# Optimization experiments

Measured on AMD Instinct MI355X. Metric: run time of the kernel, lower is better.

The kernel has to match this reference:

```python
import jax, jax.numpy as jnp
import numpy as np

NUM_HEADER = 8
DIM_HIDDEN = 512
DIM_HEADER = DIM_HIDDEN // NUM_HEADER


def setup_inputs() -> dict:
    key = jax.random.key(0)
    ks = jax.random.split(key, 11)
    B, S, D = 2, 4096, DIM_HIDDEN
    scale = 1.0 / np.sqrt(D)
    inp = {
        "q": jax.random.normal(ks[0], (B, S, D), jnp.float32),
        "k": jax.random.normal(ks[1], (B, S, D), jnp.float32),
        "v": jax.random.normal(ks[2], (B, S, D), jnp.float32),
        # nn.Linear weights are [out, in]; y = x @ W.T + b
        "Wq": jax.random.normal(ks[3], (D, D), jnp.float32) * scale,
        "bq": jax.random.normal(ks[4], (D,), jnp.float32) * scale,
        "Wk": jax.random.normal(ks[5], (D, D), jnp.float32) * scale,
        "bk": jax.random.normal(ks[6], (D,), jnp.float32) * scale,
        "Wv": jax.random.normal(ks[7], (D, D), jnp.float32) * scale,
        "bv": jax.random.normal(ks[8], (D,), jnp.float32) * scale,
        "Wo": jax.random.normal(ks[9], (D, D), jnp.float32) * scale,
        "bo": jax.random.normal(ks[10], (D,), jnp.float32) * scale,
    }
    return inp


def reference(q, k, v, Wq, bq, Wk, bk, Wv, bv, Wo, bo):
    B = q.shape[0]
    H, dh = NUM_HEADER, DIM_HEADER

    def proj(x, W, b):
        # [B,S,D] -> [B,H,S,dh]
        y = jnp.einsum('bsd,ed->bse', x, W) + b
        return y.reshape(B, -1, H, dh).transpose(0, 2, 1, 3)

    qh = proj(q, Wq, bq)
    kh = proj(k, Wk, bk)
    vh = proj(v, Wv, bv)

    scores = jnp.einsum('bhqd,bhkd->bhqk', qh, kh) / jnp.sqrt(jnp.float32(dh))
    attn = jax.nn.softmax(scores, axis=-1)
    ctx = jnp.einsum('bhqk,bhkd->bhqd', attn, vh)
    concat = ctx.transpose(0, 2, 1, 3).reshape(B, -1, H * dh)
    return jnp.einsum('bsd,ed->bse', concat, Wo) + bo
```

## Files before the change

kernel.cpp:

```cpp
#include <hip/hip_runtime.h>
#include <hip/hip_bf16.h>

typedef __attribute__((ext_vector_type(8))) short short8;
typedef __attribute__((ext_vector_type(4))) float f32x4;
typedef __attribute__((ext_vector_type(16))) float f32x16;
typedef __attribute__((ext_vector_type(4))) float f4v;

#define SEQ 4096
#define NBH 16
#define SCALE_Q 0.18033688011112042f

#define MFMA16(a, b, c) __builtin_amdgcn_mfma_f32_16x16x32_bf16(a, b, c, 0, 0, 0)
#define MFMA32(a, b, c) __builtin_amdgcn_mfma_f32_32x32x16_bf16(a, b, c, 0, 0, 0)

__device__ __forceinline__ short f2bf(float f) {
  union { float f; unsigned u; } x; x.f = f;
  unsigned r = x.u + 0x7FFFu + ((x.u >> 16) & 1u);
  return (short)(r >> 16);
}

__device__ __forceinline__ unsigned cvt_pk_bf16(float lo, float hi) {
  unsigned r;
  asm("v_cvt_pk_bf16_f32 %0, %1, %2" : "=v"(r) : "v"(lo), "v"(hi));
  return r;
}

__device__ __forceinline__ short8 cvt8(const float* __restrict__ src) {
  f4v v0 = *(const f4v*)src;
  f4v v1 = *(const f4v*)(src + 4);
  union { unsigned u[4]; short8 s; } r;
  r.u[0] = cvt_pk_bf16(v0[0], v0[1]);
  r.u[1] = cvt_pk_bf16(v0[2], v0[3]);
  r.u[2] = cvt_pk_bf16(v1[0], v1[1]);
  r.u[3] = cvt_pk_bf16(v1[2], v1[3]);
  return r.s;
}

__device__ __forceinline__ void gll16(const void* g, void* l) {
  __builtin_amdgcn_global_load_lds(
      (const __attribute__((address_space(1))) void*)g,
      (__attribute__((address_space(3))) void*)l, 16, 0, 0);
}

__device__ __forceinline__ void pswap(unsigned& a, unsigned& b) {
  asm volatile("v_permlane32_swap_b32 %0, %1" : "+v"(a), "+v"(b));
}

#define SBAR()                              \
  __builtin_amdgcn_sched_barrier(0);        \
  __builtin_amdgcn_s_barrier();             \
  __builtin_amdgcn_sched_barrier(0)

__global__ __launch_bounds__(256) void cvt_w(
    const float* __restrict__ w0, const float* __restrict__ w1,
    const float* __restrict__ w2, const float* __restrict__ w3,
    short* __restrict__ dst)
{
  int i = blockIdx.x * 256 + threadIdx.x;
  int m = i >> 15;
  int off = (i & 32767) * 8;
  const float* s = (m == 0) ? w0 : (m == 1) ? w1 : (m == 2) ? w2 : w3;
  *(short8*)(dst + (size_t)m * 262144 + off) = cvt8(s + off);
}

template <bool SWAP>
__device__ __forceinline__ void qkv_kloop(
    const float* __restrict__ Af, const short* __restrict__ W,
    char* smemA, char* smemB, f32x4 (&acc)[4][2],
    int tile_m, int tile_n, int t, int g, int q, int w)
{
  short (*As)[72] = (short(*)[72])smemA;
  for (int k0 = 0; k0 < 512; k0 += 64) {
    __syncthreads();
#pragma unroll
    for (int it = 0; it < 2; ++it) {
      int i = it * 256 + t;
      int r = i >> 3, sg = i & 7;
      *(short8*)&As[r][sg * 8] =
          cvt8(Af + (size_t)(tile_m + r) * 512 + k0 + sg * 8);
    }
#pragma unroll
    for (int it = 0; it < 4; ++it) {
      int i = it * 256 + t;
      int row = i >> 3, cg = i & 7;
      const char* gp = (const char*)W +
          ((size_t)(tile_n + row) * 512 + k0) * 2 + ((cg ^ (row & 7)) << 4);
      gll16(gp, smemB + (size_t)(it * 256 + (t & ~63)) * 16);
    }
    __syncthreads();
#pragma unroll
    for (int kk = 0; kk < 2; ++kk) {
      short8 af[4], bfv[2];
#pragma unroll
      for (int mi = 0; mi < 4; ++mi)
        af[mi] = *(const short8*)&As[mi * 16 + q][kk * 32 + g * 8];
#pragma unroll
      for (int ni = 0; ni < 2; ++ni) {
        int rB = w * 32 + ni * 16 + q;
        bfv[ni] = *(const short8*)(smemB + rB * 128 +
                                   (((4 * kk + g) ^ (rB & 7)) << 4));
      }
#pragma unroll
      for (int mi = 0; mi < 4; ++mi)
#pragma unroll
        for (int ni = 0; ni < 2; ++ni) {
          if (SWAP)
            acc[mi][ni] = MFMA16(bfv[ni], af[mi], acc[mi][ni]);
          else
            acc[mi][ni] = MFMA16(af[mi], bfv[ni], acc[mi][ni]);
        }
    }
  }
}

__global__ __launch_bounds__(256) void qkv_gemm(
    const float* __restrict__ qin, const float* __restrict__ kin,
    const float* __restrict__ vin, const short* __restrict__ Wb,
    const float* __restrict__ bq, const float* __restrict__ bk,
    const float* __restrict__ bv,
    short* __restrict__ Qh, short* __restrict__ Kh, short* __restrict__ Vt)
{
  __shared__ __align__(16) char smemA[64 * 72 * 2];
  __shared__ __align__(16) char smemB[128 * 64 * 2];
  const int t    = threadIdx.x;
  const int lane = t & 63;
  const int w    = t >> 6;
  const int g    = lane >> 4;
  const int q    = lane & 15;
  const int tile_n = blockIdx.x * 128;
  const int tile_m = blockIdx.y * 64;
  const int z      = blockIdx.z;

  const float* Af   = (z == 0) ? qin : (z == 1) ? kin : vin;
  const float* bias = (z == 0) ? bq  : (z == 1) ? bk  : bv;
  const short* W    = Wb + (size_t)z * 262144;

  f32x4 acc[4][2];
#pragma unroll
  for (int mi = 0; mi < 4; ++mi)
#pragma unroll
    for (int ni = 0; ni < 2; ++ni)
#pragma unroll
      for (int j = 0; j < 4; ++j) acc[mi][ni][j] = 0.f;

  if (z == 2)
    qkv_kloop<true>(Af, W, smemA, smemB, acc, tile_m, tile_n, t, g, q, w);
  else
    qkv_kloop<false>(Af, W, smemA, smemB, acc, tile_m, tile_n, t, g, q, w);

#pragma unroll
  for (int mi = 0; mi < 4; ++mi) {
#pragma unroll
    for (int ni = 0; ni < 2; ++ni) {
#pragma unroll
      for (int j = 0; j < 4; ++j) {
        if (z == 2) {
          int e = tile_n + w * 32 + ni * 16 + 4 * g + j;
          int srow = tile_m + mi * 16 + q;
          float val = acc[mi][ni][j] + bias[e];
          int b = srow >> 12, sl = srow & 4095;
          int h = e >> 6, d = e & 63;
          Vt[((size_t)((b * 8 + h) * 64 + d)) * SEQ + sl] = f2bf(val);
        } else {
          int m = tile_m + mi * 16 + g * 4 + j;
          int e = tile_n + w * 32 + ni * 16 + q;
          float val = acc[mi][ni][j] + bias[e];
          int b = m >> 12, s = m & 4095;
          int h = e >> 6, d = e & 63;
          size_t off = ((size_t)(b * 8 + h) * SEQ + s) * 64 + d;
          if (z == 0) Qh[off] = f2bf(val * SCALE_Q);
          else        Kh[off] = f2bf(val);
        }
      }
    }
  }
}

template <int MODE>
__global__ __launch_bounds__(256) void gemm_bt(
    const short* __restrict__ Ab,
    const short* __restrict__ Wb, const float* __restrict__ bias,
    const float* __restrict__ Opart, const float* __restrict__ lsum,
    void* __restrict__ Cout)
{
  __shared__ __align__(16) char smemA[64 * 72 * 2];
  __shared__ __align__(16) char smemB[128 * 64 * 2];
  const int t    = threadIdx.x;
  const int lane = t & 63;
  const int w    = t >> 6;
  const int g    = lane >> 4;
  const int q    = lane & 15;
  const int tile_n = blockIdx.x * 128;
  const int tile_m = blockIdx.y * 64;

  f32x4 acc[4][2];
#pragma unroll
  for (int mi = 0; mi < 4; ++mi)
#pragma unroll
    for (int ni = 0; ni < 2; ++ni)
#pragma unroll
      for (int j = 0; j < 4; ++j) acc[mi][ni][j] = 0.f;

  for (int k0 = 0; k0 < 512; k0 += 64) {
    __syncthreads();
    if (MODE == 3) {
#pragma unroll
      for (int it = 0; it < 2; ++it) {
        int i = it * 256 + t;
        int row = i >> 3, cg = i & 7;
        const char* gp = (const char*)Ab +
            ((size_t)(tile_m + row) * 512 + k0) * 2 + ((cg ^ (row & 7)) << 4);
        gll16(gp, smemA + (size_t)(it * 256 + (t & ~63)) * 16);
      }
    } else {
#pragma unroll
      for (int it = 0; it < 2; ++it) {
        int i = it * 256 + t;
        int row = i >> 3, cg = i & 7;
        int cgs = cg ^ (row & 7);
        int m = tile_m + row;
        int b = m >> 12, s = m & 4095;
        int h = k0 >> 6;
        size_t g0 = (size_t)(b * 8 + h) * SEQ + s;
        float inv = 1.0f / (lsum[g0] + lsum[g0 + (size_t)NBH * SEQ]);
        const float* o0 = Opart + g0 * 64 + cgs * 8;
        const float* o1 = Opart + (g0 + (size_t)NBH * SEQ) * 64 + cgs * 8;
        f4v a0 = *(const f4v*)o0, a1 = *(const f4v*)(o0 + 4);
        f4v b0 = *(const f4v*)o1, b1 = *(const f4v*)(o1 + 4);
        float vv[8];
#pragma unroll
        for (int j = 0; j < 4; ++j) vv[j] = (a0[j] + b0[j]) * inv;
#pragma unroll
        for (int j = 0; j < 4; ++j) vv[4 + j] = (a1[j] + b1[j]) * inv;
        union { unsigned u[4]; short8 s8; } r;
        r.u[0] = cvt_pk_bf16(vv[0], vv[1]);
        r.u[1] = cvt_pk_bf16(vv[2], vv[3]);
        r.u[2] = cvt_pk_bf16(vv[4], vv[5]);
        r.u[3] = cvt_pk_bf16(vv[6], vv[7]);
        *(short8*)(smemA + (size_t)i * 16) = r.s8;
      }
    }
#pragma unroll
    for (int it = 0; it < 4; ++it) {
      int i = it * 256 + t;
      int row = i >> 3, cg = i & 7;
      const char* gp = (const char*)Wb +
          ((size_t)(tile_n + row) * 512 + k0) * 2 + ((cg ^ (row & 7)) << 4);
      gll16(gp, smemB + (size_t)(it * 256 + (t & ~63)) * 16);
    }
    __syncthreads();
#pragma unroll
    for (int kk = 0; kk < 2; ++kk) {
      short8 af[4], bfv[2];
#pragma unroll
      for (int mi = 0; mi < 4; ++mi) {
        int rA = mi * 16 + q;
        af[mi] = *(const short8*)(smemA + rA * 128 +
                                  (((4 * kk + g) ^ (rA & 7)) << 4));
      }
#pragma unroll
      for (int ni = 0; ni < 2; ++ni) {
        int rB = w * 32 + ni * 16 + q;
        bfv[ni] = *(const short8*)(smemB + rB * 128 +
                                   (((4 * kk + g) ^ (rB & 7)) << 4));
      }
#pragma unroll
      for (int mi = 0; mi < 4; ++mi)
#pragma unroll
        for (int ni = 0; ni < 2; ++ni)
          acc[mi][ni] = MFMA16(af[mi], bfv[ni], acc[mi][ni]);
    }
  }

#pragma unroll
  for (int mi = 0; mi < 4; ++mi) {
#pragma unroll
    for (int ni = 0; ni < 2; ++ni) {
#pragma unroll
      for (int j = 0; j < 4; ++j) {
        int m = tile_m + mi * 16 + g * 4 + j;
        int e = tile_n + w * 32 + ni * 16 + q;
        ((float*)Cout)[(size_t)m * 512 + e] = acc[mi][ni][j] + bias[e];
      }
    }
  }
}

template <int NSPLIT>
__global__ __launch_bounds__(256, 4) void attn_kernel(
    const short* __restrict__ Qh, const short* __restrict__ Kh,
    const short* __restrict__ Vt, short* __restrict__ ctx,
    float* __restrict__ Opart, float* __restrict__ lsum)
{
  __shared__ __align__(16) char smem[2][16384];
  const int t    = threadIdx.x;
  const int lane = t & 63;
  const int w    = t >> 6;
  const int l31  = lane & 31;
  const int hi   = lane >> 5;

  const int fid = blockIdx.x;
  int qt, bh, split;
  if (NSPLIT == 1) {
    int lid = (fid & 7) * 64 + (fid >> 3);
    qt = lid & 31; bh = lid >> 5; split = 0;
  } else {
    int lid = (fid & 7) * 128 + (fid >> 3);
    qt = lid & 31; split = (lid >> 5) & 1; bh = lid >> 6;
  }
  const int NT  = (SEQ / 64) / NSPLIT;
  const int kt0 = split * NT;

  const size_t kbase = (size_t)bh * SEQ * 64;
  const size_t vbase = (size_t)bh * 64 * SEQ;
  const int q0 = qt * 128 + w * 32;

  short8 qf[4];
#pragma unroll
  for (int m = 0; m < 4; ++m)
    qf[m] = *(const short8*)(Qh + kbase + (size_t)(q0 + l31) * 64 + m * 16 + hi * 8);

  f32x16 fz;
#pragma unroll
  for (int r = 0; r < 16; ++r) fz[r] = 0.f;
  f32x16 acc0 = fz, acc1 = fz;
  float lrun = 0.f;

  const int rif  = lane >> 3;
  const int scol = ((lane & 7) ^ rif) * 16;
  const int xr   = (hi * 16) ^ ((lane & 7) << 4);

#define STAGE(buf, kt)                                                         \
  {                                                                            \
    _Pragma("unroll")                                                          \
    for (int i = 0; i < 4; ++i) {                                              \
      int c = w * 4 + i;                                                       \
      char* ldst = &smem[buf][c * 1024];                                       \
      if (c < 8) {                                                             \
        int row = c * 8 + rif;                                                 \
        const char* gp = (const char*)Kh +                                     \
            ((kbase + (size_t)((kt) * 64 + row) * 64) * 2 + scol);             \
        gll16(gp, ldst);                                                       \
      } else {                                                                 \
        int row = (c - 8) * 8 + rif;                                           \
        const char* gp = (const char*)Vt +                                     \
            ((vbase + (size_t)row * SEQ + (kt) * 64) * 2 + scol);              \
        gll16(gp, ldst);                                                       \
      }                                                                        \
    }                                                                          \
  }

  STAGE(0, kt0);
  int cur = 0;

  for (int it = 0; it < NT; ++it) {
    const int kt = kt0 + it;
    asm volatile("s_waitcnt vmcnt(0)" ::: "memory");
    SBAR();
    if (it < NT - 1) STAGE(cur ^ 1, kt + 1);

    const char* Kb = &smem[cur][0];
    const char* Vb = &smem[cur][8192];

    f32x16 s0, s1;
    {
      short8 k0 = *(const short8*)(Kb + (size_t)(l31) * 128 + ((32 * 0) ^ xr));
      short8 k1 = *(const short8*)(Kb + (size_t)(32 + l31) * 128 + ((32 * 0) ^ xr));
      __builtin_amdgcn_s_setprio(1);
      s0 = MFMA32(k0, qf[0], fz);
      s1 = MFMA32(k1, qf[0], fz);
      __builtin_amdgcn_s_setprio(0);
    }
#pragma unroll
    for (int m = 1; m < 4; ++m) {
      short8 k0 = *(const short8*)(Kb + (size_t)(l31) * 128 + ((32 * m) ^ xr));
      short8 k1 = *(const short8*)(Kb + (size_t)(32 + l31) * 128 + ((32 * m) ^ xr));
      __builtin_amdgcn_s_setprio(1);
      s0 = MFMA32(k0, qf[m], s0);
      s1 = MFMA32(k1, qf[m], s1);
      __builtin_amdgcn_s_setprio(0);
    }

#pragma unroll
    for (int r = 0; r < 16; ++r) s0[r] = __builtin_amdgcn_exp2f(s0[r]);
    float rs0;
    {
      float b_[8];
#pragma unroll
      for (int r = 0; r < 8; ++r) b_[r] = s0[r] + s0[r + 8];
#pragma unroll
      for (int r = 0; r < 4; ++r) b_[r] += b_[r + 4];
      rs0 = (b_[0] + b_[1]) + (b_[2] + b_[3]);
    }
    union { unsigned u[4]; short8 v; } A0c, A1c;
    {
      unsigned p0 = cvt_pk_bf16(s0[0], s0[1]);
      unsigned p1 = cvt_pk_bf16(s0[2], s0[3]);
      unsigned p2 = cvt_pk_bf16(s0[4], s0[5]);
      unsigned p3 = cvt_pk_bf16(s0[6], s0[7]);
      unsigned p4 = cvt_pk_bf16(s0[8], s0[9]);
      unsigned p5 = cvt_pk_bf16(s0[10], s0[11]);
      unsigned p6 = cvt_pk_bf16(s0[12], s0[13]);
      unsigned p7 = cvt_pk_bf16(s0[14], s0[15]);
      pswap(p0, p2); pswap(p1, p3); pswap(p4, p6); pswap(p5, p7);
      A0c.u[0] = p0; A0c.u[1] = p1; A0c.u[2] = p2; A0c.u[3] = p3;
      A1c.u[0] = p4; A1c.u[1] = p5; A1c.u[2] = p6; A1c.u[3] = p7;
    }
#pragma unroll
    for (int h2 = 0; h2 < 2; ++h2) {
      short8 pa = h2 ? A1c.v : A0c.v;
      short8 vf0 = *(const short8*)(Vb + (size_t)(l31) * 128 + ((32 * h2) ^ xr));
      short8 vf1 = *(const short8*)(Vb + (size_t)(32 + l31) * 128 + ((32 * h2) ^ xr));
      __builtin_amdgcn_s_setprio(1);
      acc0 = MFMA32(pa, vf0, acc0);
      acc1 = MFMA32(pa, vf1, acc1);
      __builtin_amdgcn_s_setprio(0);
    }

#pragma unroll
    for (int r = 0; r < 16; ++r) s1[r] = __builtin_amdgcn_exp2f(s1[r]);
    float rs1;
    {
      float b_[8];
#pragma unroll
      for (int r = 0; r < 8; ++r) b_[r] = s1[r] + s1[r + 8];
#pragma unroll
      for (int r = 0; r < 4; ++r) b_[r] += b_[r + 4];
      rs1 = (b_[0] + b_[1]) + (b_[2] + b_[3]);
    }
    {
      unsigned p0 = cvt_pk_bf16(s1[0], s1[1]);
      unsigned p1 = cvt_pk_bf16(s1[2], s1[3]);
      unsigned p2 = cvt_pk_bf16(s1[4], s1[5]);
      unsigned p3 = cvt_pk_bf16(s1[6], s1[7]);
      unsigned p4 = cvt_pk_bf16(s1[8], s1[9]);
      unsigned p5 = cvt_pk_bf16(s1[10], s1[11]);
      unsigned p6 = cvt_pk_bf16(s1[12], s1[13]);
      unsigned p7 = cvt_pk_bf16(s1[14], s1[15]);
      pswap(p0, p2); pswap(p1, p3); pswap(p4, p6); pswap(p5, p7);
      A0c.u[0] = p0; A0c.u[1] = p1; A0c.u[2] = p2; A0c.u[3] = p3;
      A1c.u[0] = p4; A1c.u[1] = p5; A1c.u[2] = p6; A1c.u[3] = p7;
    }
#pragma unroll
    for (int h2 = 0; h2 < 2; ++h2) {
      short8 pa = h2 ? A1c.v : A0c.v;
      short8 vf0 = *(const short8*)(Vb + (size_t)(l31) * 128 + ((64 + 32 * h2) ^ xr));
      short8 vf1 = *(const short8*)(Vb + (size_t)(32 + l31) * 128 + ((64 + 32 * h2) ^ xr));
      __builtin_amdgcn_s_setprio(1);
      acc0 = MFMA32(pa, vf0, acc0);
      acc1 = MFMA32(pa, vf1, acc1);
      __builtin_amdgcn_s_setprio(0);
    }

    float rs = rs0 + rs1;
    rs += __shfl_xor(rs, 32);
    lrun += rs;

    cur ^= 1;
  }

  if (NSPLIT == 1) {
    const int b = bh >> 3, hh = bh & 7;
    const float inv = 1.0f / lrun;
#pragma unroll
    for (int r = 0; r < 16; ++r) {
      int ql = (r & 3) + 8 * (r >> 2) + 4 * hi;
      float iv = __shfl(inv, ql);
      int qrow = q0 + ql;
      size_t off = ((size_t)(b * SEQ + qrow)) * 512 + hh * 64 + l31;
      ctx[off]      = f2bf(acc0[r] * iv);
      ctx[off + 32] = f2bf(acc1[r] * iv);
    }
  } else {
    float* Ob = Opart + (((size_t)(split * NBH + bh) * SEQ + q0)) * 64;
#pragma unroll
    for (int r = 0; r < 16; ++r) {
      int ql = (r & 3) + 8 * (r >> 2) + 4 * hi;
      Ob[(size_t)ql * 64 + l31]      = acc0[r];
      Ob[(size_t)ql * 64 + l31 + 32] = acc1[r];
    }
    if (hi == 0)
      lsum[(size_t)(split * NBH + bh) * SEQ + q0 + l31] = lrun;
  }
}

extern "C" void kernel_launch(void* const* d_in, const int* in_sizes, int n_in,
                              void* d_out, int out_size, void* d_ws, size_t ws_size,
                              hipStream_t stream) {
  const float* q  = (const float*)d_in[0];
  const float* k  = (const float*)d_in[1];
  const float* v  = (const float*)d_in[2];
  const float* Wq = (const float*)d_in[3];
  const float* bq = (const float*)d_in[4];
  const float* Wk = (const float*)d_in[5];
  const float* bk = (const float*)d_in[6];
  const float* Wv = (const float*)d_in[7];
  const float* bv = (const float*)d_in[8];
  const float* Wo = (const float*)d_in[9];
  const float* bo = (const float*)d_in[10];

  const size_t NELT = (size_t)NBH * SEQ * 64;
  short* Qh  = (short*)d_ws;
  short* Kh  = Qh + NELT;
  short* Vt  = Kh + NELT;
  short* ctx = Vt + NELT;
  short* Wb  = ctx + NELT;
  float* Opart = (float*)(Wb + 4 * 262144);
  float* lsum  = Opart + 2 * (size_t)NBH * SEQ * 64;
  const char* ws_end = (const char*)(lsum + 2 * (size_t)NBH * SEQ);
  const bool split2 = ws_size >= (size_t)(ws_end - (const char*)d_ws);

  dim3 tb(256);
  cvt_w<<<dim3(512), tb, 0, stream>>>(Wq, Wk, Wv, Wo, Wb);

  qkv_gemm<<<dim3(4, 128, 3), tb, 0, stream>>>(q, k, v, Wb, bq, bk, bv,
                                               Qh, Kh, Vt);
  if (split2) {
    attn_kernel<2><<<dim3(1024), tb, 0, stream>>>(Qh, Kh, Vt, ctx, Opart, lsum);
    gemm_bt<4><<<dim3(4, 128), tb, 0, stream>>>(nullptr, Wb + 786432, bo, Opart, lsum, d_out);
  } else {
    attn_kernel<1><<<dim3(512), tb, 0, stream>>>(Qh, Kh, Vt, ctx, Opart, lsum);
    gemm_bt<3><<<dim3(4, 128), tb, 0, stream>>>(ctx, Wb + 786432, bo, nullptr, nullptr, d_out);
  }
}
```

Baseline: 163.2 us.

## Split attention KV range four ways and store partial outputs in bf16

Raises the attention split-K factor from 2 to 4, launching 2048 blocks instead of 1024 so the GPU holds more parallel work. Partial outputs are now written as bf16 rather than fp32, which keeps the intermediate traffic roughly unchanged despite twice as many partials. The output projection sums four partials and their row sums. This adds combine work and a rounding step on unnormalized partial accumulators, and the workspace layout is reorganized so the partials alias the ctx buffer.

```diff
diff --git a/kernel.cpp b/kernel.cpp
--- a/kernel.cpp
+++ b/kernel.cpp
@@ -17,6 +17,12 @@
   union { float f; unsigned u; } x; x.f = f;
   unsigned r = x.u + 0x7FFFu + ((x.u >> 16) & 1u);
   return (short)(r >> 16);
+}
+
+__device__ __forceinline__ float bf2f(short s) {
+  union { unsigned u; float f; } x;
+  x.u = ((unsigned)(unsigned short)s) << 16;
+  return x.f;
 }
 
 __device__ __forceinline__ unsigned cvt_pk_bf16(float lo, float hi) {
@@ -180,7 +186,7 @@
 __global__ __launch_bounds__(256) void gemm_bt(
     const short* __restrict__ Ab,
     const short* __restrict__ Wb, const float* __restrict__ bias,
-    const float* __restrict__ Opart, const float* __restrict__ lsum,
+    const short* __restrict__ OpartB, const float* __restrict__ lsum,
     void* __restrict__ Cout)
 {
   __shared__ __align__(16) char smemA[64 * 72 * 2];
@@ -221,17 +227,24 @@
         int m = tile_m + row;
         int b = m >> 12, s = m & 4095;
         int h = k0 >> 6;
-        size_t g0 = (size_t)(b * 8 + h) * SEQ + s;
-        float inv = 1.0f / (lsum[g0] + lsum[g0 + (size_t)NBH * SEQ]);
-        const float* o0 = Opart + g0 * 64 + cgs * 8;
-        const float* o1 = Opart + (g0 + (size_t)NBH * SEQ) * 64 + cgs * 8;
-        f4v a0 = *(const f4v*)o0, a1 = *(const f4v*)(o0 + 4);
-        f4v b0 = *(const f4v*)o1, b1 = *(const f4v*)(o1 + 4);
+        size_t base = (size_t)(b * 8 + h) * SEQ + s;
+        float ltot = 0.f;
+#pragma unroll
+        for (int sp = 0; sp < 4; ++sp)
+          ltot += lsum[base + (size_t)sp * NBH * SEQ];
+        float inv = 1.0f / ltot;
         float vv[8];
 #pragma unroll
-        for (int j = 0; j < 4; ++j) vv[j] = (a0[j] + b0[j]) * inv;
-#pragma unroll
-        for (int j = 0; j < 4; ++j) vv[4 + j] = (a1[j] + b1[j]) * inv;
+        for (int j = 0; j < 8; ++j) vv[j] = 0.f;
+#pragma unroll
+        for (int sp = 0; sp < 4; ++sp) {
+          short8 o = *(const short8*)(OpartB +
+              (base + (size_t)sp * NBH * SEQ) * 64 + cgs * 8);
+#pragma unroll
+          for (int j = 0; j < 8; ++j) vv[j] += bf2f(o[j]);
+        }
+#pragma unroll
+        for (int j = 0; j < 8; ++j) vv[j] *= inv;
         union { unsigned u[4]; short8 s8; } r;
         r.u[0] = cvt_pk_bf16(vv[0], vv[1]);
         r.u[1] = cvt_pk_bf16(vv[2], vv[3]);
@@ -290,7 +303,7 @@
 __global__ __launch_bounds__(256, 4) void attn_kernel(
     const short* __restrict__ Qh, const short* __restrict__ Kh,
     const short* __restrict__ Vt, short* __restrict__ ctx,
-    float* __restrict__ Opart, float* __restrict__ lsum)
+    short* __restrict__ OpartB, float* __restrict__ lsum)
 {
   __shared__ __align__(16) char smem[2][16384];
   const int t    = threadIdx.x;
@@ -305,8 +318,8 @@
     int lid = (fid & 7) * 64 + (fid >> 3);
     qt = lid & 31; bh = lid >> 5; split = 0;
   } else {
-    int lid = (fid & 7) * 128 + (fid >> 3);
-    qt = lid & 31; split = (lid >> 5) & 1; bh = lid >> 6;
+    int lid = (fid & 7) * 256 + (fid >> 3);
+    qt = lid & 31; split = (lid >> 5) & 3; bh = lid >> 7;
   }
   const int NT  = (SEQ / 64) / NSPLIT;
   const int kt0 = split * NT;
@@ -472,12 +485,12 @@
       ctx[off + 32] = f2bf(acc1[r] * iv);
     }
   } else {
-    float* Ob = Opart + (((size_t)(split * NBH + bh) * SEQ + q0)) * 64;
+    short* Ob = OpartB + ((size_t)(split * NBH + bh) * SEQ + q0) * 64;
 #pragma unroll
     for (int r = 0; r < 16; ++r) {
       int ql = (r & 3) + 8 * (r >> 2) + 4 * hi;
-      Ob[(size_t)ql * 64 + l31]      = acc0[r];
-      Ob[(size_t)ql * 64 + l31 + 32] = acc1[r];
+      Ob[(size_t)ql * 64 + l31]      = f2bf(acc0[r]);
+      Ob[(size_t)ql * 64 + l31 + 32] = f2bf(acc1[r]);
     }
     if (hi == 0)
       lsum[(size_t)(split * NBH + bh) * SEQ + q0 + l31] = lrun;
@@ -503,23 +516,23 @@
   short* Qh  = (short*)d_ws;
   short* Kh  = Qh + NELT;
   short* Vt  = Kh + NELT;
-  short* ctx = Vt + NELT;
-  short* Wb  = ctx + NELT;
-  float* Opart = (float*)(Wb + 4 * 262144);
-  float* lsum  = Opart + 2 * (size_t)NBH * SEQ * 64;
-  const char* ws_end = (const char*)(lsum + 2 * (size_t)NBH * SEQ);
-  const bool split2 = ws_size >= (size_t)(ws_end - (const char*)d_ws);
+  short* ctx    = Vt + NELT;
+  short* OpartB = ctx;
+  short* Wb     = OpartB + 4 * NELT;
+  float* lsum   = (float*)(Wb + 4 * 262144);
+  const char* ws_end = (const char*)(lsum + 4 * (size_t)NBH * SEQ);
+  const bool split4 = ws_size >= (size_t)(ws_end - (const char*)d_ws);
 
   dim3 tb(256);
   cvt_w<<<dim3(512), tb, 0, stream>>>(Wq, Wk, Wv, Wo, Wb);
 
   qkv_gemm<<<dim3(4, 128, 3), tb, 0, stream>>>(q, k, v, Wb, bq, bk, bv,
                                                Qh, Kh, Vt);
-  if (split2) {
-    attn_kernel<2><<<dim3(1024), tb, 0, stream>>>(Qh, Kh, Vt, ctx, Opart, lsum);
-    gemm_bt<4><<<dim3(4, 128), tb, 0, stream>>>(nullptr, Wb + 786432, bo, Opart, lsum, d_out);
+  if (split4) {
+    attn_kernel<4><<<dim3(2048), tb, 0, stream>>>(Qh, Kh, Vt, ctx, OpartB, lsum);
+    gemm_bt<4><<<dim3(4, 128), tb, 0, stream>>>(nullptr, Wb + 786432, bo, OpartB, lsum, d_out);
   } else {
-    attn_kernel<1><<<dim3(512), tb, 0, stream>>>(Qh, Kh, Vt, ctx, Opart, lsum);
+    attn_kernel<1><<<dim3(512), tb, 0, stream>>>(Qh, Kh, Vt, ctx, OpartB, lsum);
     gemm_bt<3><<<dim3(4, 128), tb, 0, stream>>>(ctx, Wb + 786432, bo, nullptr, nullptr, d_out);
   }
 }
```

After: 172.3 us. 5.6% more time.
